# Performance work log

Measured on AMD Instinct MI355X. Metric: run time of the kernel, lower is better.

## Reference

```python
import jax, jax.numpy as jnp
import numpy as np

B, IN, C, HID, EMB = 1024, 512, 128, 128, 32


def setup_inputs() -> dict:
    key = jax.random.key(0)
    ks = jax.random.split(key, 9)
    s1 = 1.0 / np.sqrt(IN)
    s2 = 1.0 / np.sqrt(HID)
    return {
        "x": jax.random.normal(ks[0], (B, IN), jnp.float32),
        "pos_W1": jax.random.normal(ks[1], (C, IN, HID), jnp.float32) * s1,
        "pos_b1": jax.random.normal(ks[2], (C, HID), jnp.float32) * s1,
        "pos_W2": jax.random.normal(ks[3], (C, HID, EMB), jnp.float32) * s2,
        "pos_b2": jax.random.normal(ks[4], (C, EMB), jnp.float32) * s2,
        "neg_W1": jax.random.normal(ks[5], (C, IN, HID), jnp.float32) * s1,
        "neg_b1": jax.random.normal(ks[6], (C, HID), jnp.float32) * s1,
        "neg_W2": jax.random.normal(ks[7], (C, HID, EMB), jnp.float32) * s2,
        "neg_b2": jax.random.normal(ks[8], (C, EMB), jnp.float32) * s2,
    }


def _bank(x, W1, b1, W2, b2):
    # x: [B, IN]; W1: [C, IN, HID]; W2: [C, HID, EMB]
    h = jnp.einsum("bi,cih->bch", x, W1) + b1          # [B, C, HID]
    h = jax.nn.relu(h)                                  # dropout is identity in eval
    out = jnp.einsum("bch,che->bce", h, W2) + b2        # [B, C, EMB]
    return jnp.transpose(out, (0, 2, 1))                # [B, EMB, C]


def reference(x, pos_W1, pos_b1, pos_W2, pos_b2, neg_W1, neg_b1, neg_W2, neg_b2):
    pos = _bank(x, pos_W1, pos_b1, pos_W2, pos_b2)
    neg = _bank(x, neg_W1, neg_b1, neg_W2, neg_b2)
    return pos, neg
```

## Files before the change

### kernel.cpp

```cpp
#include <hip/hip_runtime.h>
#include <hip/hip_bf16.h>

#define B_TOT  1024
#define IN_DIM 512
#define C_DIM  128
#define HID    128
#define EMB    32
#define BK     32
#define NKT    (IN_DIM / BK)

#define WS_W1_STRIDE 65536ull
#define WS_W2_OFF    16777216ull
#define WS_X_OFF     17825792ull
#define WS_TMP_F     9175040ull
#define WS_NEEDED1_B 36700160ull
#define WS_NEEDED2_B 70254592ull

using bf16x8 = __attribute__((ext_vector_type(8))) short;
using f32x4  = __attribute__((ext_vector_type(4))) float;
using f32x2  = __attribute__((ext_vector_type(2))) float;

__device__ __forceinline__ unsigned short f2b(float f) {
    union { __hip_bfloat16 h; unsigned short u; } cv;
    cv.h = __float2bfloat16(f);
    return cv.u;
}
__device__ __forceinline__ unsigned int pack2(float a, float b) {
    return (unsigned int)f2b(a) | ((unsigned int)f2b(b) << 16);
}
__device__ __forceinline__ unsigned long long pack4(float a, float b, float c, float d) {
    return (unsigned long long)pack2(a, b) | ((unsigned long long)pack2(c, d) << 32);
}
__device__ __forceinline__ bf16x8 ld16(const unsigned short* p) {
    return *(const bf16x8*)p;
}
__device__ __forceinline__ void g2l16(const unsigned short* g, unsigned short* l) {
    __builtin_amdgcn_global_load_lds(
        (const __attribute__((address_space(1))) unsigned int*)(g),
        (__attribute__((address_space(3))) unsigned int*)(l), 16, 0, 0);
}

__global__ __launch_bounds__(256) void prepass(
    const float* __restrict__ x,
    const float* __restrict__ pW1, const float* __restrict__ pW2,
    const float* __restrict__ nW1, const float* __restrict__ nW2,
    unsigned short* __restrict__ ws)
{
    __shared__ unsigned short img[4096];
    const int blk     = blockIdx.x;
    const int pair    = blk >> 2;
    const int quarter = blk & 3;
    const int bank    = pair >> 7;
    const int c       = pair & 127;
    const int t       = threadIdx.x;

    const float* W1c = (bank ? nW1 : pW1) + (size_t)c * IN_DIM * HID;
    const float* W2c = (bank ? nW2 : pW2) + (size_t)c * HID * EMB;

    if (quarter == 0) {
        int e0 = (t & 7) * 4, h0 = (t >> 3) * 4;
        const float* src = &W2c[(size_t)h0 * EMB + e0];
        f32x4 L0 = *(const f32x4*)(src + 0 * EMB);
        f32x4 L1 = *(const f32x4*)(src + 1 * EMB);
        f32x4 L2 = *(const f32x4*)(src + 2 * EMB);
        f32x4 L3 = *(const f32x4*)(src + 3 * EMB);
        unsigned short* dst = ws + WS_W2_OFF + (size_t)pair * 4096;
#pragma unroll
        for (int j = 0; j < 4; ++j) {
            int e = e0 + j;
            int idx = (h0 >> 5) * 1024 + (e >> 4) * 512 +
                      ((((h0 & 31) >> 3) * 16 + (e & 15)) * 8) + (h0 & 7);
            *(unsigned long long*)&dst[idx] = pack4(L0[j], L1[j], L2[j], L3[j]);
        }
    }

#pragma unroll
    for (int q = 0; q < 4; ++q) {
        const int kt = quarter * 4 + q;
        const float* Wk = W1c + (size_t)kt * BK * HID;
        {
            int k0 = (t >> 5) * 4;
            int h0 = (t & 31) * 4;
            const float* src = &Wk[(size_t)k0 * HID + h0];
            f32x4 L0 = *(const f32x4*)(src + 0 * HID);
            f32x4 L1 = *(const f32x4*)(src + 1 * HID);
            f32x4 L2 = *(const f32x4*)(src + 2 * HID);
            f32x4 L3 = *(const f32x4*)(src + 3 * HID);
#pragma unroll
            for (int j = 0; j < 4; ++j) {
                int h = h0 + j;
                int idx = (h >> 4) * 512 +
                          (((k0 >> 3) * 16 + (h & 15)) * 8) + (k0 & 7);
                *(unsigned long long*)&img[idx] = pack4(L0[j], L1[j], L2[j], L3[j]);
            }
        }
        __syncthreads();
        unsigned short* dst = ws + (size_t)pair * WS_W1_STRIDE + (size_t)kt * 4096;
        *(bf16x8*)&dst[t * 16]     = *(const bf16x8*)&img[t * 16];
        *(bf16x8*)&dst[t * 16 + 8] = *(const bf16x8*)&img[t * 16 + 8];
        __syncthreads();
    }

    {
        const int row = blk;
        if (t < 128) {
            int k0 = t * 4;
            f32x4 v = *(const f32x4*)&x[(size_t)row * IN_DIM + k0];
            size_t idx = WS_X_OFF + (size_t)(row >> 7) * 65536 +
                         (size_t)(k0 >> 5) * 4096 + (size_t)((row & 127) >> 4) * 512 +
                         ((((k0 & 31) >> 3) * 16 + (row & 15)) * 8) + (k0 & 7);
            *(unsigned long long*)&ws[idx] = pack4(v[0], v[1], v[2], v[3]);
        }
    }
}

__global__ __launch_bounds__(512, 2) void bank_main(
    const float* __restrict__ pb1, const float* __restrict__ pb2,
    const float* __restrict__ nb1, const float* __restrict__ nb2,
    const unsigned short* __restrict__ ws,
    float* __restrict__ tmp,
    float* __restrict__ out)
{
    __shared__ unsigned short smem[32768];

    const int p     = blockIdx.x;
    const int xcd   = p & 7;
    const int rank  = p >> 3;
    const int cg    = rank & 7;
    const int btile = (rank >> 3) & 3;
    const int bank  = rank >> 5;
    const int c0    = xcd * 16 + cg * 2;
    const int bbase = btile * 256;

    const int t    = threadIdx.x;
    const int wave = t >> 6;
    const int lane = t & 63;
    const int lr   = lane & 15;
    const int lkg  = lane >> 4;
    const int wm   = wave >> 1;
    const int wn   = wave & 1;

    const unsigned short* xsrc0 = ws + WS_X_OFF + (size_t)(btile * 2) * 65536;
    const unsigned short* xsrc1 = xsrc0 + 65536;
    const unsigned short* wsrc0 = ws + (size_t)(bank * 128 + c0) * WS_W1_STRIDE;
    const unsigned short* wsrc1 = wsrc0 + WS_W1_STRIDE;

    f32x4 acc[4][8];
#pragma unroll
    for (int mi = 0; mi < 4; ++mi)
#pragma unroll
        for (int ni = 0; ni < 8; ++ni) acc[mi][ni] = (f32x4){0.f, 0.f, 0.f, 0.f};

#define STAGE(KT, SEL)                                                          \
    {                                                                           \
        g2l16(xsrc0 + (KT) * 4096 + t * 8, &smem[(SEL) * 8192 + t * 8]);        \
        g2l16(xsrc1 + (KT) * 4096 + t * 8, &smem[(SEL) * 8192 + 4096 + t * 8]); \
        g2l16(wsrc0 + (KT) * 4096 + t * 8, &smem[16384 + (SEL) * 8192 + t * 8]);\
        g2l16(wsrc1 + (KT) * 4096 + t * 8,                                      \
              &smem[16384 + (SEL) * 8192 + 4096 + t * 8]);                      \
    }

    STAGE(0, 0);
    __syncthreads();

    for (int kt = 0; kt < NKT; ++kt) {
        const int sel = kt & 1;
        if (kt < NKT - 1) STAGE(kt + 1, sel ^ 1);

        const unsigned short* Xb = &smem[sel * 8192 + (wm >> 1) * 4096 +
                                         (wm & 1) * 2048 + lane * 8];
        const unsigned short* Wb = &smem[16384 + sel * 8192 + wn * 4096 + lane * 8];
        bf16x8 af[4], bfr[8];
#pragma unroll
        for (int mi = 0; mi < 4; ++mi) af[mi] = ld16(Xb + mi * 512);
#pragma unroll
        for (int ni = 0; ni < 8; ++ni) bfr[ni] = ld16(Wb + ni * 512);

        __builtin_amdgcn_s_setprio(1);
#pragma unroll
        for (int mi = 0; mi < 4; ++mi)
#pragma unroll
            for (int ni = 0; ni < 8; ++ni)
                acc[mi][ni] = __builtin_amdgcn_mfma_f32_16x16x32_bf16(
                    af[mi], bfr[ni], acc[mi][ni], 0, 0, 0);
        __builtin_amdgcn_s_setprio(0);
        __syncthreads();
    }
#undef STAGE

    const int cw   = c0 + wn;
    const int pw   = bank * 128 + cw;
    const float* b1c = (bank ? nb1 : pb1) + cw * HID;
    const float* b2c = (bank ? nb2 : pb2) + cw * EMB;
    float b1v[8];
#pragma unroll
    for (int ni = 0; ni < 8; ++ni) b1v[ni] = b1c[ni * 16 + lr];
    float b2v[2];
#pragma unroll
    for (int ei = 0; ei < 2; ++ei) b2v[ei] = b2c[ei * 16 + lr];

    const unsigned short* w2base = ws + WS_W2_OFF + (size_t)pw * 4096 + lane * 8;
    bf16x8 w2f[2][4];
#pragma unroll
    for (int k2 = 0; k2 < 4; ++k2)
#pragma unroll
        for (int ei = 0; ei < 2; ++ei)
            w2f[ei][k2] = ld16(w2base + k2 * 1024 + ei * 512);

    unsigned short* slot = &smem[wave * 4096];
    f32x4 acc2[4][2];
#pragma unroll
    for (int m2 = 0; m2 < 4; ++m2)
#pragma unroll
        for (int ei = 0; ei < 2; ++ei) acc2[m2][ei] = (f32x4){0.f, 0.f, 0.f, 0.f};

#pragma unroll
    for (int ch = 0; ch < 2; ++ch) {
#pragma unroll
        for (int mi = 0; mi < 4; ++mi) {
#pragma unroll
            for (int nq = 0; nq < 4; ++nq) {
                int ni = ch * 4 + nq;
                int lh = nq * 16 + lr;
#pragma unroll
                for (int j = 0; j < 4; ++j) {
                    int r = mi * 16 + lkg * 4 + j;
                    float v = fmaxf(acc[mi][ni][j] + b1v[ni], 0.f);
                    slot[r * 64 + ((((lh >> 3) & 7) ^ (r & 7)) << 3) + (lh & 7)] = f2b(v);
                }
            }
        }
#pragma unroll
        for (int kk = 0; kk < 2; ++kk) {
            int k2 = ch * 2 + kk;
            bf16x8 a2[4];
#pragma unroll
            for (int m2 = 0; m2 < 4; ++m2) {
                int r = m2 * 16 + lr;
                a2[m2] = ld16(&slot[r * 64 + (((kk * 4 + lkg) ^ (r & 7)) << 3)]);
            }
#pragma unroll
            for (int m2 = 0; m2 < 4; ++m2)
#pragma unroll
                for (int ei = 0; ei < 2; ++ei)
                    acc2[m2][ei] = __builtin_amdgcn_mfma_f32_16x16x32_bf16(
                        a2[m2], w2f[ei][k2], acc2[m2][ei], 0, 0, 0);
        }
    }

    if (tmp != nullptr) {
        float* tb = tmp + (size_t)pw * (B_TOT * EMB);
#pragma unroll
        for (int m2 = 0; m2 < 4; ++m2) {
#pragma unroll
            for (int ei = 0; ei < 2; ++ei) {
                int e = ei * 16 + lr;
#pragma unroll
                for (int j = 0; j < 4; ++j) {
                    int brow = bbase + wm * 64 + m2 * 16 + lkg * 4 + j;
                    tb[(size_t)brow * EMB + e] = acc2[m2][ei][j] + b2v[ei];
                }
            }
        }
    } else {
        float* outb = out + (size_t)bank * B_TOT * EMB * C_DIM;
#pragma unroll
        for (int m2 = 0; m2 < 4; ++m2) {
#pragma unroll
            for (int ei = 0; ei < 2; ++ei) {
                int e = ei * 16 + lr;
#pragma unroll
                for (int j = 0; j < 4; ++j) {
                    int brow = bbase + wm * 64 + m2 * 16 + lkg * 4 + j;
                    outb[((size_t)brow * EMB + e) * C_DIM + cw] = acc2[m2][ei][j] + b2v[ei];
                }
            }
        }
    }
}

#define LP 1026
__global__ __launch_bounds__(256, 2) void untranspose(
    const float* __restrict__ tmp, float* __restrict__ out)
{
    __shared__ float lds[16 * LP];
    const int blk   = blockIdx.x;
    const int bank  = blk >> 8;
    const int cg    = (blk >> 5) & 7;
    const int chunk = blk & 31;
    const size_t beBase = (size_t)chunk * 1024;
    const int t = threadIdx.x;

#pragma unroll
    for (int ci = 0; ci < 16; ++ci) {
        const int pair = bank * 128 + cg * 16 + ci;
        f32x4 v = *(const f32x4*)&tmp[(size_t)pair * (B_TOT * EMB) + beBase + t * 4];
        *(f32x2*)&lds[ci * LP + t * 4]     = (f32x2){v[0], v[1]};
        *(f32x2*)&lds[ci * LP + t * 4 + 2] = (f32x2){v[2], v[3]};
    }
    __syncthreads();

    float* outb = out + (size_t)bank * (B_TOT * EMB * C_DIM);
#pragma unroll
    for (int w = 0; w < 16; ++w) {
        int be = w * 64 + (t >> 2);
        int c4 = t & 3;
        f32x4 o;
#pragma unroll
        for (int j = 0; j < 4; ++j) o[j] = lds[(c4 * 4 + j) * LP + be];
        *(f32x4*)&outb[(beBase + be) * C_DIM + cg * 16 + c4 * 4] = o;
    }
}
#undef LP

#define XS_LD 68
#define W1_LD 68
#define HS_LD 132
#define W2_LD 132
__device__ __forceinline__ bf16x8 load8u(const unsigned short* p) {
    union { unsigned long long q[2]; bf16x8 v; } u;
    u.q[0] = *(const unsigned long long*)(p);
    u.q[1] = *(const unsigned long long*)(p + 4);
    return u.v;
}
__global__ __launch_bounds__(256, 2) void bank_fallback(
    const float* __restrict__ x,
    const float* __restrict__ pW1, const float* __restrict__ pb1,
    const float* __restrict__ pW2, const float* __restrict__ pb2,
    const float* __restrict__ nW1, const float* __restrict__ nb1,
    const float* __restrict__ nW2, const float* __restrict__ nb2,
    float* __restrict__ out)
{
    __shared__ unsigned short Xs [128][XS_LD];
    __shared__ unsigned short W1T[HID][W1_LD];
    __shared__ unsigned short Hs [128][HS_LD];
    __shared__ unsigned short W2T[EMB][W2_LD];
    int p = blockIdx.x;
    int xcd = p & 7, rank = p >> 3;
    int c = xcd * 16 + (rank & 15);
    int btile = (rank >> 4) & 7;
    int bank = rank >> 7;
    int bbase = btile * 128;
    const float* W1c = (bank ? nW1 : pW1) + (size_t)c * IN_DIM * HID;
    const float* b1c = (bank ? nb1 : pb1) + c * HID;
    const float* W2c = (bank ? nW2 : pW2) + (size_t)c * HID * EMB;
    const float* b2c = (bank ? nb2 : pb2) + c * EMB;
    float* outb = out + (size_t)bank * B_TOT * EMB * C_DIM;
    int t = threadIdx.x, wave = t >> 6, lane = t & 63;
    int lr = lane & 15, lkg = lane >> 4, wm = wave >> 1, wn = wave & 1;
    {
        int e0 = (t & 7) * 4, h0 = (t >> 3) * 4;
        f32x4 L0 = *(const f32x4*)&W2c[(h0 + 0) * EMB + e0];
        f32x4 L1 = *(const f32x4*)&W2c[(h0 + 1) * EMB + e0];
        f32x4 L2 = *(const f32x4*)&W2c[(h0 + 2) * EMB + e0];
        f32x4 L3 = *(const f32x4*)&W2c[(h0 + 3) * EMB + e0];
#pragma unroll
        for (int j = 0; j < 4; ++j)
            *(unsigned long long*)&W2T[e0 + j][h0] = pack4(L0[j], L1[j], L2[j], L3[j]);
    }
    float b1v[4];
#pragma unroll
    for (int ni = 0; ni < 4; ++ni) b1v[ni] = b1c[wn * 64 + ni * 16 + lr];
    float b2v[2];
#pragma unroll
    for (int ei = 0; ei < 2; ++ei) b2v[ei] = b2c[ei * 16 + lr];
    f32x4 acc[4][4];
#pragma unroll
    for (int mi = 0; mi < 4; ++mi)
#pragma unroll
        for (int ni = 0; ni < 4; ++ni) acc[mi][ni] = (f32x4){0.f, 0.f, 0.f, 0.f};
    for (int kt = 0; kt < 8; ++kt) {
        int kb = kt * 64;
#pragma unroll
        for (int w8 = 0; w8 < 8; ++w8) {
            int f = w8 * 256 + t;
            int row = f >> 4, col = (f & 15) * 4;
            f32x4 v = *(const f32x4*)&x[(size_t)(bbase + row) * IN_DIM + kb + col];
            *(unsigned long long*)&Xs[row][col] = pack4(v[0], v[1], v[2], v[3]);
        }
#pragma unroll
        for (int g = 0; g < 2; ++g) {
            int s = g * 256 + t;
            int k0 = (s >> 5) * 4, h0 = (s & 31) * 4;
            const float* src = &W1c[(size_t)(kb + k0) * HID + h0];
            f32x4 L0 = *(const f32x4*)(src + 0 * HID);
            f32x4 L1 = *(const f32x4*)(src + 1 * HID);
            f32x4 L2 = *(const f32x4*)(src + 2 * HID);
            f32x4 L3 = *(const f32x4*)(src + 3 * HID);
#pragma unroll
            for (int j = 0; j < 4; ++j)
                *(unsigned long long*)&W1T[h0 + j][k0] = pack4(L0[j], L1[j], L2[j], L3[j]);
        }
        __syncthreads();
#pragma unroll
        for (int ki = 0; ki < 2; ++ki) {
            int kcol = ki * 32 + lkg * 8;
            bf16x8 af[4], bfr[4];
#pragma unroll
            for (int mi = 0; mi < 4; ++mi) af[mi] = load8u(&Xs[wm * 64 + mi * 16 + lr][kcol]);
#pragma unroll
            for (int ni = 0; ni < 4; ++ni) bfr[ni] = load8u(&W1T[wn * 64 + ni * 16 + lr][kcol]);
#pragma unroll
            for (int mi = 0; mi < 4; ++mi)
#pragma unroll
                for (int ni = 0; ni < 4; ++ni)
                    acc[mi][ni] = __builtin_amdgcn_mfma_f32_16x16x32_bf16(
                        af[mi], bfr[ni], acc[mi][ni], 0, 0, 0);
        }
        __syncthreads();
    }
#pragma unroll
    for (int mi = 0; mi < 4; ++mi) {
        int row = wm * 64 + mi * 16 + lkg * 4;
#pragma unroll
        for (int ni = 0; ni < 4; ++ni) {
            int col = wn * 64 + ni * 16 + lr;
#pragma unroll
            for (int j = 0; j < 4; ++j)
                Hs[row + j][col] = f2b(fmaxf(acc[mi][ni][j] + b1v[ni], 0.f));
        }
    }
    __syncthreads();
    f32x4 acc2[2][2];
#pragma unroll
    for (int m2 = 0; m2 < 2; ++m2)
#pragma unroll
        for (int ei = 0; ei < 2; ++ei) acc2[m2][ei] = (f32x4){0.f, 0.f, 0.f, 0.f};
    int rb = wave * 32;
#pragma unroll
    for (int k2 = 0; k2 < 4; ++k2) {
        int kcol = k2 * 32 + lkg * 8;
        bf16x8 a2[2], b2f[2];
#pragma unroll
        for (int m2 = 0; m2 < 2; ++m2) a2[m2] = load8u(&Hs[rb + m2 * 16 + lr][kcol]);
#pragma unroll
        for (int ei = 0; ei < 2; ++ei) b2f[ei] = load8u(&W2T[ei * 16 + lr][kcol]);
#pragma unroll
        for (int m2 = 0; m2 < 2; ++m2)
#pragma unroll
            for (int ei = 0; ei < 2; ++ei)
                acc2[m2][ei] = __builtin_amdgcn_mfma_f32_16x16x32_bf16(
                    a2[m2], b2f[ei], acc2[m2][ei], 0, 0, 0);
    }
#pragma unroll
    for (int m2 = 0; m2 < 2; ++m2)
#pragma unroll
        for (int ei = 0; ei < 2; ++ei) {
            int e = ei * 16 + lr;
#pragma unroll
            for (int j = 0; j < 4; ++j) {
                int brow = bbase + rb + m2 * 16 + lkg * 4 + j;
                outb[((size_t)brow * EMB + e) * C_DIM + c] = acc2[m2][ei][j] + b2v[ei];
            }
        }
}

extern "C" void kernel_launch(void* const* d_in, const int* in_sizes, int n_in,
                              void* d_out, int out_size, void* d_ws, size_t ws_size,
                              hipStream_t stream) {
    const float* x   = (const float*)d_in[0];
    const float* pW1 = (const float*)d_in[1];
    const float* pb1 = (const float*)d_in[2];
    const float* pW2 = (const float*)d_in[3];
    const float* pb2 = (const float*)d_in[4];
    const float* nW1 = (const float*)d_in[5];
    const float* nb1 = (const float*)d_in[6];
    const float* nW2 = (const float*)d_in[7];
    const float* nb2 = (const float*)d_in[8];
    float* out = (float*)d_out;

    if (ws_size >= WS_NEEDED2_B) {
        unsigned short* ws = (unsigned short*)d_ws;
        float* tmp = (float*)d_ws + WS_TMP_F;
        prepass<<<dim3(1024), dim3(256), 0, stream>>>(x, pW1, pW2, nW1, nW2, ws);
        bank_main<<<dim3(512), dim3(512), 0, stream>>>(pb1, pb2, nb1, nb2, ws, tmp, out);
        untranspose<<<dim3(512), dim3(256), 0, stream>>>(tmp, out);
    } else if (ws_size >= WS_NEEDED1_B) {
        unsigned short* ws = (unsigned short*)d_ws;
        prepass<<<dim3(1024), dim3(256), 0, stream>>>(x, pW1, pW2, nW1, nW2, ws);
        bank_main<<<dim3(512), dim3(512), 0, stream>>>(pb1, pb2, nb1, nb2, ws,
                                                       (float*)nullptr, out);
    } else {
        bank_fallback<<<dim3(2048), dim3(256), 0, stream>>>(
            x, pW1, pb1, pW2, pb2, nW1, nb1, nW2, nb2, out);
    }
}
```

Before: 71.25 us.

## Prefetch two k-tiles ahead with explicit waitcnt and barriers

Restructures the GEMM1 main loop into a fully unrolled sequence. Fragments are read from LDS into registers first, then a barrier is taken, and only after that is the buffer just consumed refilled with tile kt+2. Global-to-LDS loads therefore stay in flight two steps ahead, and completion is tracked with s_waitcnt vmcnt instead of a blanket __syncthreads. The goal is to hide global load latency behind the MFMA work. In exchange it hand-manages vmcnt counts and adds a second barrier per step, which is fragile if the instruction count per stage changes.

```diff
diff --git a/kernel.cpp b/kernel.cpp
--- a/kernel.cpp
+++ b/kernel.cpp
@@ -160,32 +160,50 @@
               &smem[16384 + (SEL) * 8192 + 4096 + t * 8]);                      \
     }
 
-    STAGE(0, 0);
-    __syncthreads();
-
-    for (int kt = 0; kt < NKT; ++kt) {
-        const int sel = kt & 1;
-        if (kt < NKT - 1) STAGE(kt + 1, sel ^ 1);
-
-        const unsigned short* Xb = &smem[sel * 8192 + (wm >> 1) * 4096 +
-                                         (wm & 1) * 2048 + lane * 8];
-        const unsigned short* Wb = &smem[16384 + sel * 8192 + wn * 4096 + lane * 8];
-        bf16x8 af[4], bfr[8];
-#pragma unroll
-        for (int mi = 0; mi < 4; ++mi) af[mi] = ld16(Xb + mi * 512);
-#pragma unroll
-        for (int ni = 0; ni < 8; ++ni) bfr[ni] = ld16(Wb + ni * 512);
-
-        __builtin_amdgcn_s_setprio(1);
-#pragma unroll
-        for (int mi = 0; mi < 4; ++mi)
-#pragma unroll
-            for (int ni = 0; ni < 8; ++ni)
-                acc[mi][ni] = __builtin_amdgcn_mfma_f32_16x16x32_bf16(
-                    af[mi], bfr[ni], acc[mi][ni], 0, 0, 0);
-        __builtin_amdgcn_s_setprio(0);
-        __syncthreads();
-    }
+#define KSTEP(KT, DOSTAGE, VM)                                                  \
+    {                                                                           \
+        const int sel_ = (KT) & 1;                                              \
+        const unsigned short* Xb = &smem[sel_ * 8192 + (wm >> 1) * 4096 +       \
+                                         (wm & 1) * 2048 + lane * 8];           \
+        const unsigned short* Wb = &smem[16384 + sel_ * 8192 + wn * 4096 +      \
+                                         lane * 8];                             \
+        bf16x8 af[4], bfr[8];                                                   \
+        _Pragma("unroll")                                                       \
+        for (int i = 0; i < 4; ++i) af[i] = ld16(Xb + i * 512);                 \
+        _Pragma("unroll")                                                       \
+        for (int n = 0; n < 8; ++n) bfr[n] = ld16(Wb + n * 512);                \
+        asm volatile("s_waitcnt lgkmcnt(0)" ::: "memory");                      \
+        __builtin_amdgcn_sched_barrier(0);                                      \
+        __builtin_amdgcn_s_barrier();                                           \
+        __builtin_amdgcn_sched_barrier(0);                                      \
+        if (DOSTAGE) { STAGE((KT) + 2, sel_) }                                  \
+        __builtin_amdgcn_sched_barrier(0);                                      \
+        __builtin_amdgcn_s_setprio(1);                                          \
+        _Pragma("unroll")                                                       \
+        for (int mi = 0; mi < 4; ++mi)                                          \
+            _Pragma("unroll")                                                   \
+            for (int ni = 0; ni < 8; ++ni)                                      \
+                acc[mi][ni] = __builtin_amdgcn_mfma_f32_16x16x32_bf16(          \
+                    af[mi], bfr[ni], acc[mi][ni], 0, 0, 0);                     \
+        __builtin_amdgcn_s_setprio(0);                                          \
+        asm volatile("s_waitcnt vmcnt(" #VM ")" ::: "memory");                  \
+        __builtin_amdgcn_sched_barrier(0);                                      \
+        __builtin_amdgcn_s_barrier();                                           \
+        __builtin_amdgcn_sched_barrier(0);                                      \
+    }
+
+    STAGE(0, 0)
+    STAGE(1, 1)
+    asm volatile("s_waitcnt vmcnt(4)" ::: "memory");
+    __builtin_amdgcn_sched_barrier(0);
+    __builtin_amdgcn_s_barrier();
+    __builtin_amdgcn_sched_barrier(0);
+
+    KSTEP(0, 1, 4)  KSTEP(1, 1, 4)  KSTEP(2, 1, 4)  KSTEP(3, 1, 4)
+    KSTEP(4, 1, 4)  KSTEP(5, 1, 4)  KSTEP(6, 1, 4)  KSTEP(7, 1, 4)
+    KSTEP(8, 1, 4)  KSTEP(9, 1, 4)  KSTEP(10, 1, 4) KSTEP(11, 1, 4)
+    KSTEP(12, 1, 4) KSTEP(13, 1, 4) KSTEP(14, 0, 0) KSTEP(15, 0, 0)
+#undef KSTEP
 #undef STAGE
 
     const int cw   = c0 + wn;
```

After: 72.79 us. 2.2% more time.
